# Kernel tuning notes

Measured on AMD Instinct MI355X. Metric: run time of the kernel, lower is better.

Reference implementation:

```python
import jax, jax.numpy as jnp
import numpy as np

N = 100      # num sensors/nodes
C = 32       # channels (hard-coded in module)
H = 512      # hidden_size (hard-coded)
T = 64       # window_size (lags)
B = 16       # batch
E = 2000     # edges = N * topk
HORIZON = 10


def _arma(x, ei, ew, W, V, b, n):
    # ARMAConv, num_stacks=1, num_layers=1, GELU act, dropout off (eval)
    h = x @ W                                    # (n, C)
    row, col = ei[0], ei[1]
    deg = jax.ops.segment_sum(ew, col, num_segments=n)
    dinv = jnp.where(deg > 0, 1.0 / jnp.sqrt(jnp.maximum(deg, 1e-12)), 0.0)
    norm = dinv[row] * ew * dinv[col]            # gcn_norm, no self loops
    agg = jax.ops.segment_sum(norm[:, None] * h[row], col, num_segments=n)
    return jax.nn.gelu(agg + x @ V + b, approximate=False)


def _lstm_step(h, c, xt, Wih, Whh, bih, bhh):
    g = xt @ Wih.T + h @ Whh.T + bih + bhh
    i, f, gg, o = jnp.split(g, 4, axis=-1)       # torch gate order i,f,g,o
    c = jax.nn.sigmoid(f) * c + jax.nn.sigmoid(i) * jnp.tanh(gg)
    h = jax.nn.sigmoid(o) * jnp.tanh(c)
    return h, c


def _lstm_layer(xs, Wih, Whh, bih, bhh):
    # xs: (T, B, in) -> outputs (T, B, H), final h
    Bn = xs.shape[1]
    init = (jnp.zeros((Bn, H), xs.dtype), jnp.zeros((Bn, H), xs.dtype))
    def step(carry, xt):
        hc = _lstm_step(carry[0], carry[1], xt, Wih, Whh, bih, bhh)
        return hc, hc[0]
    (hT, cT), hs = jax.lax.scan(step, init, xs)
    return hs, hT


def setup_inputs() -> dict:
    key = jax.random.key(0)
    ks = jax.random.split(key, 20)
    s = 0.05
    def nrm(k, shape):
        return jax.random.normal(k, shape, jnp.float32) * s
    ei = jax.random.randint(ks[1], (2, E), 0, N)
    ei = ei.at[0, 0].set(N - 1).at[1, 0].set(N - 1)  # ensure max node id present
    z = lambda *sh: jnp.zeros(sh, jnp.float32)
    return {
        "window": jax.random.normal(ks[0], (B * N, T), jnp.float32),
        "edge_index": ei,
        "edge_attr": jax.random.uniform(ks[2], (E,), jnp.float32),
        "W_embed": nrm(ks[3], (N, C)),
        "tg_w": nrm(ks[4], (1, C)), "tg_v": nrm(ks[5], (1, C)), "tg_b": z(C),
        "gnn_w": nrm(ks[6], (1, C)), "gnn_v": nrm(ks[7], (1, C)), "gnn_b": z(C),
        "lstm_Wih0": nrm(ks[8], (4 * H, N * C)), "lstm_Whh0": nrm(ks[9], (4 * H, H)),
        "lstm_bih0": z(4 * H), "lstm_bhh0": z(4 * H),
        "lstm_Wih1": nrm(ks[10], (4 * H, H)), "lstm_Whh1": nrm(ks[11], (4 * H, H)),
        "lstm_bih1": z(4 * H), "lstm_bhh1": z(4 * H),
        "c1_Wih": nrm(ks[12], (4 * H, N * C)), "c1_Whh": nrm(ks[13], (4 * H, H)),
        "c1_bih": z(4 * H), "c1_bhh": z(4 * H),
        "c2_Wih": nrm(ks[14], (4 * H, H)), "c2_Whh": nrm(ks[15], (4 * H, H)),
        "c2_bih": z(4 * H), "c2_bhh": z(4 * H),
        "Wp": nrm(ks[16], (N, H)), "bp": z(N),
    }


def _forward(edge_index, window, edge_attr, W_embed, tg_w, tg_v, tg_b,
             gnn_w, gnn_v, gnn_b,
             lstm_Wih0, lstm_Whh0, lstm_bih0, lstm_bhh0,
             lstm_Wih1, lstm_Whh1, lstm_bih1, lstm_bhh1,
             c1_Wih, c1_Whh, c1_bih, c1_bhh,
             c2_Wih, c2_Whh, c2_bih, c2_bhh, Wp, bp):
    BN = B * N
    # batch edges over B (offset b*N), exactly as the torch offset arithmetic
    bi = (edge_index[:, None, :] + (jnp.arange(B) * N)[None, :, None]).reshape(2, B * E)
    battr = jnp.tile(edge_attr, B)
    # temporal batching inside TGConv: offsets t*(B*N) on node-major flat x
    ti = (bi[:, None, :] + (jnp.arange(T) * BN)[None, :, None]).reshape(2, T * B * E)
    tattr = jnp.tile(battr, T)
    x = _arma(window.reshape(BN * T, 1), ti, tattr, tg_w, tg_v, tg_b, BN * T)  # (BN*T, C)
    x = x.reshape(B, N, T, C).transpose(0, 2, 1, 3) + W_embed                 # (B,T,N,C)
    x = x.reshape(B, T, N * C).transpose(1, 0, 2)                             # (T,B,NC)
    hs0, h1f = _lstm_layer(x, lstm_Wih0, lstm_Whh0, lstm_bih0, lstm_bhh0)
    hs1, h2f = _lstm_layer(hs0, lstm_Wih1, lstm_Whh1, lstm_bih1, lstm_bhh1)
    # original assigns (h_n, h_n): cell states seeded from hidden states
    def step(carry, _):
        h1, c1, h2, c2 = carry
        pred = h2 @ Wp.T + bp                      # (B, N)
        g = _arma(pred.reshape(BN, 1), bi, battr, gnn_w, gnn_v, gnn_b, BN)
        xin = (g.reshape(B, N, C) + W_embed).reshape(B, N * C)
        h1n, c1n = _lstm_step(h1, c1, xin, c1_Wih, c1_Whh, c1_bih, c1_bhh)
        h2n, c2n = _lstm_step(h2, c2, h1n, c2_Wih, c2_Whh, c2_bih, c2_bhh)
        return (h1n, c1n, h2n, c2n), pred.reshape(-1)
    _, preds = jax.lax.scan(step, (h1f, h1f, h2f, h2f), None, length=HORIZON)
    return preds.T                                  # (B*N, HORIZON)


def reference(window, edge_index, edge_attr, W_embed, tg_w, tg_v, tg_b,
              gnn_w, gnn_v, gnn_b,
              lstm_Wih0, lstm_Whh0, lstm_bih0, lstm_bhh0,
              lstm_Wih1, lstm_Whh1, lstm_bih1, lstm_bhh1,
              c1_Wih, c1_Whh, c1_bih, c1_bhh,
              c2_Wih, c2_Whh, c2_bih, c2_bhh, Wp, bp):
    return _forward(edge_index, window, edge_attr, W_embed, tg_w, tg_v, tg_b,
                    gnn_w, gnn_v, gnn_b,
                    lstm_Wih0, lstm_Whh0, lstm_bih0, lstm_bhh0,
                    lstm_Wih1, lstm_Whh1, lstm_bih1, lstm_bhh1,
                    c1_Wih, c1_Whh, c1_bih, c1_bhh,
                    c2_Wih, c2_Whh, c2_bih, c2_bhh, Wp, bp)
```

## Files before the change

kernel.cpp:

```cpp
#include <hip/hip_runtime.h>
#include <math.h>

#define TT 64
#define HZN 10
#define NBLK 256

__device__ __forceinline__ float sigm(float x) { return 1.f / (1.f + expf(-x)); }
__device__ __forceinline__ float gelu_f(float x) { return 0.5f * x * (1.f + erff(x * 0.70710678118654752f)); }

__device__ __forceinline__ float cLd(const float* p) {
  return __hip_atomic_load(p, __ATOMIC_RELAXED, __HIP_MEMORY_SCOPE_AGENT);
}
__device__ __forceinline__ void cSt(float* p, float v) {
  __hip_atomic_store(p, v, __ATOMIC_RELAXED, __HIP_MEMORY_SCOPE_AGENT);
}

__device__ __forceinline__ void gbar(unsigned* flags, unsigned* gen,
                                     int bid, int tid, unsigned& bgen) {
  ++bgen;
  __syncthreads();
  if (bid == 0) {
    if (tid > 0 && tid < NBLK) {
      while (__hip_atomic_load(&flags[tid], __ATOMIC_RELAXED, __HIP_MEMORY_SCOPE_AGENT) < bgen)
        __builtin_amdgcn_s_sleep(1);
    }
    __syncthreads();
    if (tid == 0)
      __hip_atomic_store(gen, bgen, __ATOMIC_RELAXED, __HIP_MEMORY_SCOPE_AGENT);
  } else {
    if (tid == 0) {
      asm volatile("s_waitcnt vmcnt(0)" ::: "memory");
      __hip_atomic_store(&flags[bid], bgen, __ATOMIC_RELAXED, __HIP_MEMORY_SCOPE_AGENT);
      while (__hip_atomic_load(gen, __ATOMIC_RELAXED, __HIP_MEMORY_SCOPE_AGENT) < bgen)
        __builtin_amdgcn_s_sleep(1);
    }
    __syncthreads();
  }
}

__device__ __forceinline__ void red32(float (&a)[4][4]) {
#pragma unroll
  for (int q = 0; q < 4; ++q)
#pragma unroll
    for (int r = 0; r < 4; ++r) {
      float v = a[q][r];
      v += __shfl_xor(v, 16); v += __shfl_xor(v, 8); v += __shfl_xor(v, 4);
      v += __shfl_xor(v, 2);  v += __shfl_xor(v, 1);
      a[q][r] = v;
    }
}

__device__ __forceinline__ void red64(float (&a)[4][4]) {
#pragma unroll
  for (int q = 0; q < 4; ++q)
#pragma unroll
    for (int r = 0; r < 4; ++r) {
      float v = a[q][r];
      v += __shfl_xor(v, 32); v += __shfl_xor(v, 16); v += __shfl_xor(v, 8);
      v += __shfl_xor(v, 4);  v += __shfl_xor(v, 2);  v += __shfl_xor(v, 1);
      a[q][r] = v;
    }
}

__global__ void setup_kernel(const int* __restrict__ ei, const float* __restrict__ ew,
                             int* __restrict__ cptr, int* __restrict__ csrc, float* __restrict__ cnorm) {
  __shared__ float deg[100];
  __shared__ float dinv[100];
  __shared__ int cnt[100];
  __shared__ int pos[100];
  __shared__ int ptr[101];
  const int t = threadIdx.x;
  if (t < 100) { deg[t] = 0.f; cnt[t] = 0; }
  __syncthreads();
  for (int e = t; e < 2000; e += 256) {
    int c = ei[2000 + e];
    atomicAdd(&deg[c], ew[e]);
    atomicAdd(&cnt[c], 1);
  }
  __syncthreads();
  if (t < 100) dinv[t] = (deg[t] > 0.f) ? 1.f / sqrtf(fmaxf(deg[t], 1e-12f)) : 0.f;
  if (t == 0) {
    ptr[0] = 0;
    for (int n = 0; n < 100; ++n) ptr[n + 1] = ptr[n] + cnt[n];
  }
  __syncthreads();
  if (t < 100) pos[t] = ptr[t];
  if (t < 101) cptr[t] = ptr[t];
  __syncthreads();
  for (int e = t; e < 2000; e += 256) {
    int r = ei[e], c = ei[2000 + e];
    int p = atomicAdd(&pos[c], 1);
    csrc[p] = r;
    cnorm[p] = dinv[r] * ew[e] * dinv[c];
  }
}

__global__ void xs_kernel(const float* __restrict__ win,
                          const int* __restrict__ cptr, const int* __restrict__ csrc,
                          const float* __restrict__ cnorm,
                          const float* __restrict__ tgw, const float* __restrict__ tgv,
                          const float* __restrict__ tgb, const float* __restrict__ Wemb,
                          float* __restrict__ XS) {
  const int g = blockIdx.x * 256 + threadIdx.x;
  if (g >= 102400) return;
  const int n2 = g % 100;
  const int base = g - n2;
  float s = 0.f;
  const int p0 = cptr[n2], p1 = cptr[n2 + 1];
  for (int p = p0; p < p1; ++p) s += cnorm[p] * win[base + csrc[p]];
  const float x = win[g];
  const int t = g % 64;
  const int bb = g / 6400;
  const int n = (g / 64) % 100;
  float* dst = XS + (size_t)(t * 16 + bb) * 3200 + n * 32;
  for (int c = 0; c < 32; ++c) {
    float v = s * tgw[c] + x * tgv[c] + tgb[c];
    dst[c] = gelu_f(v) + Wemb[n * 32 + c];
  }
}

__global__ __launch_bounds__(256) void g0_gemm(const float* __restrict__ XS, const float* __restrict__ W,
                                               const float* __restrict__ b1, const float* __restrict__ b2,
                                               float* __restrict__ G0) {
  __shared__ float As[16][68];
  __shared__ float Bs[16][68];
  const int tid = threadIdx.x;
  const int m0 = blockIdx.y * 64, n0 = blockIdx.x * 64;
  const int tx = tid & 15, ty = tid >> 4;
  const int lr = tid >> 2, lk = (tid & 3) * 4;
  float acc[4][4] = {};
  for (int k0 = 0; k0 < 3200; k0 += 16) {
    float4 av = *(const float4*)&XS[(size_t)(m0 + lr) * 3200 + k0 + lk];
    float4 bv = *(const float4*)&W[(size_t)(n0 + lr) * 3200 + k0 + lk];
    As[lk + 0][lr] = av.x; As[lk + 1][lr] = av.y; As[lk + 2][lr] = av.z; As[lk + 3][lr] = av.w;
    Bs[lk + 0][lr] = bv.x; Bs[lk + 1][lr] = bv.y; Bs[lk + 2][lr] = bv.z; Bs[lk + 3][lr] = bv.w;
    __syncthreads();
#pragma unroll
    for (int kk = 0; kk < 16; ++kk) {
      float4 a = *(const float4*)&As[kk][ty * 4];
      float4 b = *(const float4*)&Bs[kk][tx * 4];
      acc[0][0] += a.x * b.x; acc[0][1] += a.x * b.y; acc[0][2] += a.x * b.z; acc[0][3] += a.x * b.w;
      acc[1][0] += a.y * b.x; acc[1][1] += a.y * b.y; acc[1][2] += a.y * b.z; acc[1][3] += a.y * b.w;
      acc[2][0] += a.z * b.x; acc[2][1] += a.z * b.y; acc[2][2] += a.z * b.z; acc[2][3] += a.z * b.w;
      acc[3][0] += a.w * b.x; acc[3][1] += a.w * b.y; acc[3][2] += a.w * b.z; acc[3][3] += a.w * b.w;
    }
    __syncthreads();
  }
#pragma unroll
  for (int i = 0; i < 4; ++i) {
    const int m = m0 + ty * 4 + i;
#pragma unroll
    for (int j = 0; j < 4; ++j) {
      const int nn = n0 + tx * 4 + j;
      G0[(size_t)m * 2048 + nn] = acc[i][j] + b1[nn] + b2[nn];
    }
  }
}

struct CoopArgs {
  const float* G0;
  const float* Whh0;
  const float* Wih1; const float* Whh1; const float* bih1; const float* bhh1;
  const float* c1Wih; const float* c1Whh; const float* c1bih; const float* c1bhh;
  const float* c2Wih; const float* c2Whh; const float* c2bih; const float* c2bhh;
  const float* Wp; const float* bp;
  const float* gw; const float* gv; const float* gb;
  const float* Wemb;
  const int* cptr; const int* csrc; const float* cnorm;
  float* hs0; float* hL1; float* c0; float* cL1;
  float* h1d; float* c1b; float* h2d; float* c2b;
  float* pred; float* xin;
  unsigned* flags; unsigned* gen;
  float* out;
};

__global__ __launch_bounds__(512, 2) void coop_kernel(CoopArgs A) {
  __shared__ float lds[16384];
  const int tid = threadIdx.x;
  const int bid = blockIdx.x;
  const int gid = bid * 512 + tid;
  unsigned bgen = 0;

  const int layer = bid >> 7;
  const int ublk = bid & 127;
  const int u0 = ublk * 4;
  const int bg = tid >> 7;
  const int du = (tid >> 5) & 3;
  const int s = tid & 31;
  const int n_s = u0 + du;

  for (int t2 = 0; t2 <= TT; ++t2) {
    if (layer == 0) {
      if (t2 < TT) {
        const int t0 = t2;
        float acc[4][4] = {};
        if (t0 > 0) {
          const float* src = A.hs0 + (size_t)(t0 - 1) * 8192;
          for (int i = tid; i < 8192; i += 512) lds[i] = cLd(&src[i]);
        }
        __syncthreads();
        if (t0 > 0) {
          for (int jj = 0; jj < 16; ++jj) {
            const int j = jj * 32 + s;
            const float w0 = A.Whh0[(n_s) * 512 + j];
            const float w1 = A.Whh0[(512 + n_s) * 512 + j];
            const float w2 = A.Whh0[(1024 + n_s) * 512 + j];
            const float w3 = A.Whh0[(1536 + n_s) * 512 + j];
#pragma unroll
            for (int br = 0; br < 4; ++br) {
              const float hv = lds[(bg * 4 + br) * 512 + j];
              acc[0][br] += w0 * hv; acc[1][br] += w1 * hv;
              acc[2][br] += w2 * hv; acc[3][br] += w3 * hv;
            }
          }
        }
        red32(acc);
        if (s == 0) {
#pragma unroll
          for (int br = 0; br < 4; ++br) {
            const int b = bg * 4 + br;
            const float* g0r = A.G0 + (size_t)(t0 * 16 + b) * 2048;
            const float gi = acc[0][br] + g0r[n_s];
            const float gf = acc[1][br] + g0r[512 + n_s];
            const float gg = acc[2][br] + g0r[1024 + n_s];
            const float go = acc[3][br] + g0r[1536 + n_s];
            const float cp = (t0 > 0) ? A.c0[b * 512 + n_s] : 0.f;
            const float cn = sigm(gf) * cp + sigm(gi) * tanhf(gg);
            const float hn = sigm(go) * tanhf(cn);
            A.c0[b * 512 + n_s] = cn;
            cSt(&A.hs0[(size_t)t0 * 8192 + b * 512 + n_s], hn);
          }
        }
      }
    } else {
      if (t2 >= 1) {
        const int t1 = t2 - 1;
        float acc[4][4] = {};
        {
          const float* sA = A.hs0 + (size_t)t1 * 8192;
          for (int i = tid; i < 8192; i += 512) lds[i] = cLd(&sA[i]);
          if (t1 > 0) {
            const float* sB = A.hL1 + (t1 & 1) * 8192;
            for (int i = tid; i < 8192; i += 512) lds[8192 + i] = cLd(&sB[i]);
          }
        }
        __syncthreads();
        for (int jj = 0; jj < 16; ++jj) {
          const int j = jj * 32 + s;
          const float wa0 = A.Wih1[(n_s) * 512 + j];
          const float wa1 = A.Wih1[(512 + n_s) * 512 + j];
          const float wa2 = A.Wih1[(1024 + n_s) * 512 + j];
          const float wa3 = A.Wih1[(1536 + n_s) * 512 + j];
#pragma unroll
          for (int br = 0; br < 4; ++br) {
            const float ha = lds[(bg * 4 + br) * 512 + j];
            acc[0][br] += wa0 * ha; acc[1][br] += wa1 * ha;
            acc[2][br] += wa2 * ha; acc[3][br] += wa3 * ha;
          }
          if (t1 > 0) {
            const float wb0 = A.Whh1[(n_s) * 512 + j];
            const float wb1 = A.Whh1[(512 + n_s) * 512 + j];
            const float wb2 = A.Whh1[(1024 + n_s) * 512 + j];
            const float wb3 = A.Whh1[(1536 + n_s) * 512 + j];
#pragma unroll
            for (int br = 0; br < 4; ++br) {
              const float hb = lds[8192 + (bg * 4 + br) * 512 + j];
              acc[0][br] += wb0 * hb; acc[1][br] += wb1 * hb;
              acc[2][br] += wb2 * hb; acc[3][br] += wb3 * hb;
            }
          }
        }
        red32(acc);
        if (s == 0) {
#pragma unroll
          for (int br = 0; br < 4; ++br) {
            const int b = bg * 4 + br;
            const float gi = acc[0][br] + A.bih1[n_s] + A.bhh1[n_s];
            const float gf = acc[1][br] + A.bih1[512 + n_s] + A.bhh1[512 + n_s];
            const float gg = acc[2][br] + A.bih1[1024 + n_s] + A.bhh1[1024 + n_s];
            const float go = acc[3][br] + A.bih1[1536 + n_s] + A.bhh1[1536 + n_s];
            const float cp = (t1 > 0) ? A.cL1[b * 512 + n_s] : 0.f;
            const float cn = sigm(gf) * cp + sigm(gi) * tanhf(gg);
            const float hn = sigm(go) * tanhf(cn);
            A.cL1[b * 512 + n_s] = cn;
            cSt(&A.hL1[((t1 & 1) ^ 1) * 8192 + b * 512 + n_s], hn);
          }
        }
      }
    }
    gbar(A.flags, A.gen, bid, tid, bgen);
  }

  if (gid < 8192) {
    const float h1v = cLd(&A.hs0[(size_t)63 * 8192 + gid]);
    cSt(&A.h1d[gid], h1v); cSt(&A.c1b[gid], h1v);
    const float h2v = cLd(&A.hL1[gid]);
    cSt(&A.h2d[gid], h2v); cSt(&A.c2b[gid], h2v);
  }
  gbar(A.flags, A.gen, bid, tid, bgen);

  for (int hz = 0; hz < HZN; ++hz) {
    const int cur = hz & 1, nxt = cur ^ 1;

    if (gid < 25600) {
      const int bn = gid >> 4, sp = gid & 15;
      const int b = bn / 100, n = bn % 100;
      const float* h2 = A.h2d + cur * 8192 + b * 512;
      const float* wp = A.Wp + n * 512;
      float a = 0.f;
      for (int jj = 0; jj < 32; ++jj) { const int j = jj * 16 + sp; a += cLd(&h2[j]) * wp[j]; }
      a += __shfl_xor(a, 1); a += __shfl_xor(a, 2); a += __shfl_xor(a, 4); a += __shfl_xor(a, 8);
      if (sp == 0) {
        const float v = a + A.bp[n];
        cSt(&A.pred[bn], v);
        A.out[bn * HZN + hz] = v;
      }
    }
    gbar(A.flags, A.gen, bid, tid, bgen);

    if (bid < 100) {
      for (int i = tid; i < 1600; i += 512) lds[i] = cLd(&A.pred[i]);
      __syncthreads();
      const int g2 = bid * 512 + tid;
      const int b = g2 / 3200, rem = g2 % 3200;
      const int n = rem >> 5, c = rem & 31;
      float s2 = 0.f;
      const int p0 = A.cptr[n], p1 = A.cptr[n + 1];
      for (int p = p0; p < p1; ++p) s2 += A.cnorm[p] * lds[b * 100 + A.csrc[p]];
      const float pv = lds[b * 100 + n];
      const float v = s2 * A.gw[c] + pv * A.gv[c] + A.gb[c];
      cSt(&A.xin[g2], gelu_f(v) + A.Wemb[n * 32 + c]);
    }
    gbar(A.flags, A.gen, bid, tid, bgen);

    {
      const int uc = bid & 63, bq = bid >> 6;
      const int u = tid >> 6, sl = tid & 63;
      const int n = uc * 8 + u;
      float* xinl = lds;
      float* h1l = lds + 12800;
      for (int i = tid; i < 12800; i += 512) xinl[i] = cLd(&A.xin[(size_t)bq * 12800 + i]);
      for (int i = tid; i < 2048; i += 512) h1l[i] = cLd(&A.h1d[cur * 8192 + bq * 2048 + i]);
      __syncthreads();
      float acc[4][4] = {};
      for (int jj = 0; jj < 50; ++jj) {
        const int j = jj * 64 + sl;
        const float w0 = A.c1Wih[(size_t)(n) * 3200 + j];
        const float w1 = A.c1Wih[(size_t)(512 + n) * 3200 + j];
        const float w2 = A.c1Wih[(size_t)(1024 + n) * 3200 + j];
        const float w3 = A.c1Wih[(size_t)(1536 + n) * 3200 + j];
#pragma unroll
        for (int bl = 0; bl < 4; ++bl) {
          const float xv = xinl[bl * 3200 + j];
          acc[0][bl] += w0 * xv; acc[1][bl] += w1 * xv;
          acc[2][bl] += w2 * xv; acc[3][bl] += w3 * xv;
        }
      }
      for (int jj = 0; jj < 8; ++jj) {
        const int j = jj * 64 + sl;
        const float w0 = A.c1Whh[(n) * 512 + j];
        const float w1 = A.c1Whh[(512 + n) * 512 + j];
        const float w2 = A.c1Whh[(1024 + n) * 512 + j];
        const float w3 = A.c1Whh[(1536 + n) * 512 + j];
#pragma unroll
        for (int bl = 0; bl < 4; ++bl) {
          const float hv = h1l[bl * 512 + j];
          acc[0][bl] += w0 * hv; acc[1][bl] += w1 * hv;
          acc[2][bl] += w2 * hv; acc[3][bl] += w3 * hv;
        }
      }
      red64(acc);
      if (sl == 0) {
#pragma unroll
        for (int bl = 0; bl < 4; ++bl) {
          const int b = bq * 4 + bl;
          const float gi = acc[0][bl] + A.c1bih[n] + A.c1bhh[n];
          const float gf = acc[1][bl] + A.c1bih[512 + n] + A.c1bhh[512 + n];
          const float gg = acc[2][bl] + A.c1bih[1024 + n] + A.c1bhh[1024 + n];
          const float go = acc[3][bl] + A.c1bih[1536 + n] + A.c1bhh[1536 + n];
          const float cp = cLd(&A.c1b[b * 512 + n]);
          const float cn = sigm(gf) * cp + sigm(gi) * tanhf(gg);
          const float hn = sigm(go) * tanhf(cn);
          cSt(&A.c1b[b * 512 + n], cn);
          cSt(&A.h1d[nxt * 8192 + b * 512 + n], hn);
        }
      }
    }
    gbar(A.flags, A.gen, bid, tid, bgen);

    {
      const int uc = bid & 63, bq = bid >> 6;
      const int u = tid >> 6, sl = tid & 63;
      const int n = uc * 8 + u;
      float* hAl = lds;
      float* hBl = lds + 2048;
      for (int i = tid; i < 2048; i += 512) {
        hAl[i] = cLd(&A.h1d[nxt * 8192 + bq * 2048 + i]);
        hBl[i] = cLd(&A.h2d[cur * 8192 + bq * 2048 + i]);
      }
      __syncthreads();
      float acc[4][4] = {};
      for (int jj = 0; jj < 8; ++jj) {
        const int j = jj * 64 + sl;
        const float wa0 = A.c2Wih[(n) * 512 + j];
        const float wa1 = A.c2Wih[(512 + n) * 512 + j];
        const float wa2 = A.c2Wih[(1024 + n) * 512 + j];
        const float wa3 = A.c2Wih[(1536 + n) * 512 + j];
        const float wb0 = A.c2Whh[(n) * 512 + j];
        const float wb1 = A.c2Whh[(512 + n) * 512 + j];
        const float wb2 = A.c2Whh[(1024 + n) * 512 + j];
        const float wb3 = A.c2Whh[(1536 + n) * 512 + j];
#pragma unroll
        for (int bl = 0; bl < 4; ++bl) {
          const float ha = hAl[bl * 512 + j];
          const float hb = hBl[bl * 512 + j];
          acc[0][bl] += wa0 * ha + wb0 * hb;
          acc[1][bl] += wa1 * ha + wb1 * hb;
          acc[2][bl] += wa2 * ha + wb2 * hb;
          acc[3][bl] += wa3 * ha + wb3 * hb;
        }
      }
      red64(acc);
      if (sl == 0) {
#pragma unroll
        for (int bl = 0; bl < 4; ++bl) {
          const int b = bq * 4 + bl;
          const float gi = acc[0][bl] + A.c2bih[n] + A.c2bhh[n];
          const float gf = acc[1][bl] + A.c2bih[512 + n] + A.c2bhh[512 + n];
          const float gg = acc[2][bl] + A.c2bih[1024 + n] + A.c2bhh[1024 + n];
          const float go = acc[3][bl] + A.c2bih[1536 + n] + A.c2bhh[1536 + n];
          const float cp = cLd(&A.c2b[b * 512 + n]);
          const float cn = sigm(gf) * cp + sigm(gi) * tanhf(gg);
          const float hn = sigm(go) * tanhf(cn);
          cSt(&A.c2b[b * 512 + n], cn);
          cSt(&A.h2d[nxt * 8192 + b * 512 + n], hn);
        }
      }
    }
    gbar(A.flags, A.gen, bid, tid, bgen);
  }
}

extern "C" void kernel_launch(void* const* d_in, const int* in_sizes, int n_in,
                              void* d_out, int out_size, void* d_ws, size_t ws_size,
                              hipStream_t stream) {
  (void)in_sizes; (void)n_in; (void)out_size; (void)ws_size;
  const float* window = (const float*)d_in[0];
  const int* ei = (const int*)d_in[1];
  const float* ew = (const float*)d_in[2];
  const float* Wemb = (const float*)d_in[3];
  const float* tgw = (const float*)d_in[4];
  const float* tgv = (const float*)d_in[5];
  const float* tgb = (const float*)d_in[6];
  const float* gw = (const float*)d_in[7];
  const float* gv = (const float*)d_in[8];
  const float* gb = (const float*)d_in[9];
  const float* Wih0 = (const float*)d_in[10];
  const float* Whh0 = (const float*)d_in[11];
  const float* bih0 = (const float*)d_in[12];
  const float* bhh0 = (const float*)d_in[13];
  const float* Wih1 = (const float*)d_in[14];
  const float* Whh1 = (const float*)d_in[15];
  const float* bih1 = (const float*)d_in[16];
  const float* bhh1 = (const float*)d_in[17];
  const float* c1Wih = (const float*)d_in[18];
  const float* c1Whh = (const float*)d_in[19];
  const float* c1bih = (const float*)d_in[20];
  const float* c1bhh = (const float*)d_in[21];
  const float* c2Wih = (const float*)d_in[22];
  const float* c2Whh = (const float*)d_in[23];
  const float* c2bih = (const float*)d_in[24];
  const float* c2bhh = (const float*)d_in[25];
  const float* Wp = (const float*)d_in[26];
  const float* bp = (const float*)d_in[27];

  char* w = (char*)d_ws;
  size_t off = 0;
  auto alloc = [&](size_t bytes) { void* p = w + off; off = (off + bytes + 255) & ~(size_t)255; return p; };
  int* cptr = (int*)alloc(101 * 4);
  int* csrc = (int*)alloc(2000 * 4);
  float* cnorm = (float*)alloc(2000 * 4);
  float* XS = (float*)alloc((size_t)1024 * 3200 * 4);
  float* G0 = (float*)alloc((size_t)1024 * 2048 * 4);
  float* hs0 = (float*)alloc((size_t)64 * 8192 * 4);
  float* hL1 = (float*)alloc((size_t)2 * 8192 * 4);
  float* c0 = (float*)alloc((size_t)8192 * 4);
  float* cL1 = (float*)alloc((size_t)8192 * 4);
  float* h1d = (float*)alloc((size_t)2 * 8192 * 4);
  float* c1b = (float*)alloc((size_t)8192 * 4);
  float* h2d = (float*)alloc((size_t)2 * 8192 * 4);
  float* c2b = (float*)alloc((size_t)8192 * 4);
  float* pred = (float*)alloc(1600 * 4);
  float* xin = (float*)alloc((size_t)51200 * 4);
  unsigned* flags = (unsigned*)alloc(NBLK * 4);
  unsigned* gen = (unsigned*)alloc(64);

  hipMemsetAsync(flags, 0, NBLK * 4, stream);
  hipMemsetAsync(gen, 0, 4, stream);

  setup_kernel<<<1, 256, 0, stream>>>(ei, ew, cptr, csrc, cnorm);
  xs_kernel<<<400, 256, 0, stream>>>(window, cptr, csrc, cnorm, tgw, tgv, tgb, Wemb, XS);
  g0_gemm<<<dim3(32, 16), 256, 0, stream>>>(XS, Wih0, bih0, bhh0, G0);

  CoopArgs A;
  A.G0 = G0; A.Whh0 = Whh0;
  A.Wih1 = Wih1; A.Whh1 = Whh1; A.bih1 = bih1; A.bhh1 = bhh1;
  A.c1Wih = c1Wih; A.c1Whh = c1Whh; A.c1bih = c1bih; A.c1bhh = c1bhh;
  A.c2Wih = c2Wih; A.c2Whh = c2Whh; A.c2bih = c2bih; A.c2bhh = c2bhh;
  A.Wp = Wp; A.bp = bp; A.gw = gw; A.gv = gv; A.gb = gb; A.Wemb = Wemb;
  A.cptr = cptr; A.csrc = csrc; A.cnorm = cnorm;
  A.hs0 = hs0; A.hL1 = hL1; A.c0 = c0; A.cL1 = cL1;
  A.h1d = h1d; A.c1b = c1b; A.h2d = h2d; A.c2b = c2b;
  A.pred = pred; A.xin = xin;
  A.flags = flags; A.gen = gen;
  A.out = (float*)d_out;
  void* params[] = { &A };
  hipLaunchCooperativeKernel(coop_kernel, dim3(NBLK), dim3(512), params, 0, stream);
}
```

Baseline: 1.900 ms.

## Split encoder/decoder kernels, use all-to-all flag barrier, compute preds redundantly per block

Replaces the master-block gather/release grid barrier with a flat barrier where every block publishes its flag and polls all others, removing one serialised hop per barrier. Splits the cooperative kernel into a scan kernel and a decoder kernel, dropping the handoff barrier and using plain stores for state owned by one thread. In the decoder, each block recomputes the projection and graph conv for its batch quarter in LDS, cutting two grid barriers per horizon step. The cost is redundant projection/GNN work in every block and heavier flag polling traffic.

```diff
diff --git a/kernel.cpp b/kernel.cpp
--- a/kernel.cpp
+++ b/kernel.cpp
@@ -15,27 +15,16 @@
   __hip_atomic_store(p, v, __ATOMIC_RELAXED, __HIP_MEMORY_SCOPE_AGENT);
 }
 
-__device__ __forceinline__ void gbar(unsigned* flags, unsigned* gen,
-                                     int bid, int tid, unsigned& bgen) {
+__device__ __forceinline__ void gbar(unsigned* flags, int bid, int tid, unsigned& bgen) {
   ++bgen;
   __syncthreads();
-  if (bid == 0) {
-    if (tid > 0 && tid < NBLK) {
-      while (__hip_atomic_load(&flags[tid], __ATOMIC_RELAXED, __HIP_MEMORY_SCOPE_AGENT) < bgen)
-        __builtin_amdgcn_s_sleep(1);
-    }
-    __syncthreads();
-    if (tid == 0)
-      __hip_atomic_store(gen, bgen, __ATOMIC_RELAXED, __HIP_MEMORY_SCOPE_AGENT);
-  } else {
-    if (tid == 0) {
-      asm volatile("s_waitcnt vmcnt(0)" ::: "memory");
-      __hip_atomic_store(&flags[bid], bgen, __ATOMIC_RELAXED, __HIP_MEMORY_SCOPE_AGENT);
-      while (__hip_atomic_load(gen, __ATOMIC_RELAXED, __HIP_MEMORY_SCOPE_AGENT) < bgen)
-        __builtin_amdgcn_s_sleep(1);
-    }
-    __syncthreads();
-  }
+  if (tid == 0)
+    __hip_atomic_store(&flags[bid], bgen, __ATOMIC_RELAXED, __HIP_MEMORY_SCOPE_AGENT);
+  if (tid < NBLK) {
+    while (__hip_atomic_load(&flags[tid], __ATOMIC_RELAXED, __HIP_MEMORY_SCOPE_AGENT) < bgen)
+      __builtin_amdgcn_s_sleep(2);
+  }
+  __syncthreads();
 }
 
 __device__ __forceinline__ void red32(float (&a)[4][4]) {
@@ -157,24 +146,16 @@
   }
 }
 
-struct CoopArgs {
+struct ScanArgs {
   const float* G0;
   const float* Whh0;
   const float* Wih1; const float* Whh1; const float* bih1; const float* bhh1;
-  const float* c1Wih; const float* c1Whh; const float* c1bih; const float* c1bhh;
-  const float* c2Wih; const float* c2Whh; const float* c2bih; const float* c2bhh;
-  const float* Wp; const float* bp;
-  const float* gw; const float* gv; const float* gb;
-  const float* Wemb;
-  const int* cptr; const int* csrc; const float* cnorm;
   float* hs0; float* hL1; float* c0; float* cL1;
   float* h1d; float* c1b; float* h2d; float* c2b;
-  float* pred; float* xin;
-  unsigned* flags; unsigned* gen;
-  float* out;
+  unsigned* flags;
 };
 
-__global__ __launch_bounds__(512, 2) void coop_kernel(CoopArgs A) {
+__global__ __launch_bounds__(512, 2) void scan_kernel(ScanArgs A) {
   __shared__ float lds[16384];
   const int tid = threadIdx.x;
   const int bid = blockIdx.x;
@@ -288,60 +269,85 @@
         }
       }
     }
-    gbar(A.flags, A.gen, bid, tid, bgen);
+    gbar(A.flags, bid, tid, bgen);
   }
 
   if (gid < 8192) {
     const float h1v = cLd(&A.hs0[(size_t)63 * 8192 + gid]);
-    cSt(&A.h1d[gid], h1v); cSt(&A.c1b[gid], h1v);
+    A.h1d[gid] = h1v; A.c1b[gid] = h1v;
     const float h2v = cLd(&A.hL1[gid]);
-    cSt(&A.h2d[gid], h2v); cSt(&A.c2b[gid], h2v);
-  }
-  gbar(A.flags, A.gen, bid, tid, bgen);
+    A.h2d[gid] = h2v; A.c2b[gid] = h2v;
+  }
+}
+
+struct DecArgs {
+  const float* c1Wih; const float* c1Whh; const float* c1bih; const float* c1bhh;
+  const float* c2Wih; const float* c2Whh; const float* c2bih; const float* c2bhh;
+  const float* Wp; const float* bp;
+  const float* gw; const float* gv; const float* gb;
+  const float* Wemb;
+  const int* cptr; const int* csrc; const float* cnorm;
+  float* h1d; float* c1b; float* h2d; float* c2b;
+  unsigned* flags;
+  float* out;
+};
+
+__global__ __launch_bounds__(512, 2) void dec_kernel(DecArgs A) {
+  __shared__ float lds[15360];
+  float* xinl = lds;
+  float* h1l = lds + 12800;
+  float* predl = lds + 14848;
+  const int tid = threadIdx.x;
+  const int bid = blockIdx.x;
+  unsigned bgen = 0;
+
+  const int uc = bid & 63, bq = bid >> 6;
+  const int u = tid >> 6, sl = tid & 63;
+  const int n = uc * 8 + u;
 
   for (int hz = 0; hz < HZN; ++hz) {
     const int cur = hz & 1, nxt = cur ^ 1;
 
-    if (gid < 25600) {
-      const int bn = gid >> 4, sp = gid & 15;
-      const int b = bn / 100, n = bn % 100;
-      const float* h2 = A.h2d + cur * 8192 + b * 512;
-      const float* wp = A.Wp + n * 512;
-      float a = 0.f;
-      for (int jj = 0; jj < 32; ++jj) { const int j = jj * 16 + sp; a += cLd(&h2[j]) * wp[j]; }
-      a += __shfl_xor(a, 1); a += __shfl_xor(a, 2); a += __shfl_xor(a, 4); a += __shfl_xor(a, 8);
-      if (sp == 0) {
-        const float v = a + A.bp[n];
-        cSt(&A.pred[bn], v);
-        A.out[bn * HZN + hz] = v;
-      }
-    }
-    gbar(A.flags, A.gen, bid, tid, bgen);
-
-    if (bid < 100) {
-      for (int i = tid; i < 1600; i += 512) lds[i] = cLd(&A.pred[i]);
-      __syncthreads();
-      const int g2 = bid * 512 + tid;
-      const int b = g2 / 3200, rem = g2 % 3200;
-      const int n = rem >> 5, c = rem & 31;
+    for (int i = tid; i < 2048; i += 512) {
+      xinl[i] = cLd(&A.h2d[cur * 8192 + bq * 2048 + i]);
+      h1l[i] = cLd(&A.h1d[cur * 8192 + bq * 2048 + i]);
+    }
+    __syncthreads();
+    {
+      const int d00 = tid >> 4, sp = tid & 15;
+      for (int pass = 0; pass < 13; ++pass) {
+        const int d = pass * 32 + d00;
+        if (d < 400) {
+          const int pb = d / 100, pn = d - pb * 100;
+          const float* h2r = xinl + pb * 512;
+          const float* wpr = A.Wp + pn * 512;
+          float a = 0.f;
+          for (int jj = 0; jj < 32; ++jj) { const int j = jj * 16 + sp; a += h2r[j] * wpr[j]; }
+          a += __shfl_xor(a, 1); a += __shfl_xor(a, 2); a += __shfl_xor(a, 4); a += __shfl_xor(a, 8);
+          if (sp == 0) predl[d] = a + A.bp[pn];
+        }
+      }
+    }
+    __syncthreads();
+    if (uc == 0) {
+      for (int i = tid; i < 400; i += 512) {
+        const int bl = i / 100, n2 = i - bl * 100;
+        A.out[((bq * 4 + bl) * 100 + n2) * HZN + hz] = predl[i];
+      }
+    }
+    for (int k = 0; k < 25; ++k) {
+      const int idx = k * 512 + tid;
+      const int bl = idx / 3200, rem = idx - bl * 3200;
+      const int n2 = rem >> 5, c = rem & 31;
       float s2 = 0.f;
-      const int p0 = A.cptr[n], p1 = A.cptr[n + 1];
-      for (int p = p0; p < p1; ++p) s2 += A.cnorm[p] * lds[b * 100 + A.csrc[p]];
-      const float pv = lds[b * 100 + n];
+      const int p0 = A.cptr[n2], p1 = A.cptr[n2 + 1];
+      for (int p = p0; p < p1; ++p) s2 += A.cnorm[p] * predl[bl * 100 + A.csrc[p]];
+      const float pv = predl[bl * 100 + n2];
       const float v = s2 * A.gw[c] + pv * A.gv[c] + A.gb[c];
-      cSt(&A.xin[g2], gelu_f(v) + A.Wemb[n * 32 + c]);
-    }
-    gbar(A.flags, A.gen, bid, tid, bgen);
-
+      xinl[idx] = gelu_f(v) + A.Wemb[n2 * 32 + c];
+    }
+    __syncthreads();
     {
-      const int uc = bid & 63, bq = bid >> 6;
-      const int u = tid >> 6, sl = tid & 63;
-      const int n = uc * 8 + u;
-      float* xinl = lds;
-      float* h1l = lds + 12800;
-      for (int i = tid; i < 12800; i += 512) xinl[i] = cLd(&A.xin[(size_t)bq * 12800 + i]);
-      for (int i = tid; i < 2048; i += 512) h1l[i] = cLd(&A.h1d[cur * 8192 + bq * 2048 + i]);
-      __syncthreads();
       float acc[4][4] = {};
       for (int jj = 0; jj < 50; ++jj) {
         const int j = jj * 64 + sl;
@@ -378,20 +384,17 @@
           const float gf = acc[1][bl] + A.c1bih[512 + n] + A.c1bhh[512 + n];
           const float gg = acc[2][bl] + A.c1bih[1024 + n] + A.c1bhh[1024 + n];
           const float go = acc[3][bl] + A.c1bih[1536 + n] + A.c1bhh[1536 + n];
-          const float cp = cLd(&A.c1b[b * 512 + n]);
+          const float cp = A.c1b[b * 512 + n];
           const float cn = sigm(gf) * cp + sigm(gi) * tanhf(gg);
           const float hn = sigm(go) * tanhf(cn);
-          cSt(&A.c1b[b * 512 + n], cn);
+          A.c1b[b * 512 + n] = cn;
           cSt(&A.h1d[nxt * 8192 + b * 512 + n], hn);
         }
       }
     }
-    gbar(A.flags, A.gen, bid, tid, bgen);
+    gbar(A.flags, bid, tid, bgen);
 
     {
-      const int uc = bid & 63, bq = bid >> 6;
-      const int u = tid >> 6, sl = tid & 63;
-      const int n = uc * 8 + u;
       float* hAl = lds;
       float* hBl = lds + 2048;
       for (int i = tid; i < 2048; i += 512) {
@@ -429,15 +432,15 @@
           const float gf = acc[1][bl] + A.c2bih[512 + n] + A.c2bhh[512 + n];
           const float gg = acc[2][bl] + A.c2bih[1024 + n] + A.c2bhh[1024 + n];
           const float go = acc[3][bl] + A.c2bih[1536 + n] + A.c2bhh[1536 + n];
-          const float cp = cLd(&A.c2b[b * 512 + n]);
+          const float cp = A.c2b[b * 512 + n];
           const float cn = sigm(gf) * cp + sigm(gi) * tanhf(gg);
           const float hn = sigm(go) * tanhf(cn);
-          cSt(&A.c2b[b * 512 + n], cn);
+          A.c2b[b * 512 + n] = cn;
           cSt(&A.h2d[nxt * 8192 + b * 512 + n], hn);
         }
       }
     }
-    gbar(A.flags, A.gen, bid, tid, bgen);
+    gbar(A.flags, bid, tid, bgen);
   }
 }
 
@@ -490,30 +493,32 @@
   float* c1b = (float*)alloc((size_t)8192 * 4);
   float* h2d = (float*)alloc((size_t)2 * 8192 * 4);
   float* c2b = (float*)alloc((size_t)8192 * 4);
-  float* pred = (float*)alloc(1600 * 4);
-  float* xin = (float*)alloc((size_t)51200 * 4);
-  unsigned* flags = (unsigned*)alloc(NBLK * 4);
-  unsigned* gen = (unsigned*)alloc(64);
-
-  hipMemsetAsync(flags, 0, NBLK * 4, stream);
-  hipMemsetAsync(gen, 0, 4, stream);
+  unsigned* flags1 = (unsigned*)alloc(NBLK * 4);
+  unsigned* flags2 = (unsigned*)alloc(NBLK * 4);
+
+  hipMemsetAsync(flags1, 0, NBLK * 4 * 2, stream);
 
   setup_kernel<<<1, 256, 0, stream>>>(ei, ew, cptr, csrc, cnorm);
   xs_kernel<<<400, 256, 0, stream>>>(window, cptr, csrc, cnorm, tgw, tgv, tgb, Wemb, XS);
   g0_gemm<<<dim3(32, 16), 256, 0, stream>>>(XS, Wih0, bih0, bhh0, G0);
 
-  CoopArgs A;
-  A.G0 = G0; A.Whh0 = Whh0;
-  A.Wih1 = Wih1; A.Whh1 = Whh1; A.bih1 = bih1; A.bhh1 = bhh1;
-  A.c1Wih = c1Wih; A.c1Whh = c1Whh; A.c1bih = c1bih; A.c1bhh = c1bhh;
-  A.c2Wih = c2Wih; A.c2Whh = c2Whh; A.c2bih = c2bih; A.c2bhh = c2bhh;
-  A.Wp = Wp; A.bp = bp; A.gw = gw; A.gv = gv; A.gb = gb; A.Wemb = Wemb;
-  A.cptr = cptr; A.csrc = csrc; A.cnorm = cnorm;
-  A.hs0 = hs0; A.hL1 = hL1; A.c0 = c0; A.cL1 = cL1;
-  A.h1d = h1d; A.c1b = c1b; A.h2d = h2d; A.c2b = c2b;
-  A.pred = pred; A.xin = xin;
-  A.flags = flags; A.gen = gen;
-  A.out = (float*)d_out;
-  void* params[] = { &A };
-  hipLaunchCooperativeKernel(coop_kernel, dim3(NBLK), dim3(512), params, 0, stream);
-}
+  ScanArgs S;
+  S.G0 = G0; S.Whh0 = Whh0;
+  S.Wih1 = Wih1; S.Whh1 = Whh1; S.bih1 = bih1; S.bhh1 = bhh1;
+  S.hs0 = hs0; S.hL1 = hL1; S.c0 = c0; S.cL1 = cL1;
+  S.h1d = h1d; S.c1b = c1b; S.h2d = h2d; S.c2b = c2b;
+  S.flags = flags1;
+  void* sp[] = { &S };
+  hipLaunchCooperativeKernel(scan_kernel, dim3(NBLK), dim3(512), sp, 0, stream);
+
+  DecArgs D;
+  D.c1Wih = c1Wih; D.c1Whh = c1Whh; D.c1bih = c1bih; D.c1bhh = c1bhh;
+  D.c2Wih = c2Wih; D.c2Whh = c2Whh; D.c2bih = c2bih; D.c2bhh = c2bhh;
+  D.Wp = Wp; D.bp = bp; D.gw = gw; D.gv = gv; D.gb = gb; D.Wemb = Wemb;
+  D.cptr = cptr; D.csrc = csrc; D.cnorm = cnorm;
+  D.h1d = h1d; D.c1b = c1b; D.h2d = h2d; D.c2b = c2b;
+  D.flags = flags2;
+  D.out = (float*)d_out;
+  void* dp[] = { &D };
+  hipLaunchCooperativeKernel(dec_kernel, dim3(NBLK), dim3(512), dp, 0, stream);
+}
```

Result: slower. 3.043 ms (+60.2%).
